# Optimization experiments

Measured on AMD Instinct MI355X. Metric: run time of the kernel, lower is better.

Reference implementation:

```python
import jax, jax.numpy as jnp
import numpy as np

# --- static config (matches init_kwargs / input_specs) ---
N_GRAPHS = 32
NODES = 1000          # num_nodes per graph
N = N_GRAPHS * NODES  # 32000 total nodes
F_IN = 128            # num_features
E_DIM = 16            # edge_attr_dim
H, C = 4, 16          # heads, GAT_dim
HC = H * C            # 64
E = 512000            # edges (before self-loops)
PROJ = 8              # proj_nodes
OUT = 256             # output_dim
NEG_SLOPE = 0.2       # PyG GATConv default


def setup_inputs() -> dict:
    key = jax.random.key(0)
    ks = jax.random.split(key, 20)
    s = 0.1
    return {
        "x": jax.random.normal(ks[0], (N, F_IN), jnp.float32),
        "edge_attr": jax.random.normal(ks[1], (E, E_DIM), jnp.float32),
        # layer 0 (input_conv): F_IN -> H*C
        "W0":   jax.random.normal(ks[2], (F_IN, HC), jnp.float32) * s,
        "a_s0": jax.random.normal(ks[3], (H, C), jnp.float32) * s,
        "a_d0": jax.random.normal(ks[4], (H, C), jnp.float32) * s,
        "W_e0": jax.random.normal(ks[5], (E_DIM, HC), jnp.float32) * s,
        "a_e0": jax.random.normal(ks[6], (H, C), jnp.float32) * s,
        "b0":   jnp.zeros((HC,), jnp.float32),
        # layers 1..2 stacked: HC -> H*C
        "Wg":   jax.random.normal(ks[7], (2, HC, HC), jnp.float32) * s,
        "a_sg": jax.random.normal(ks[8], (2, H, C), jnp.float32) * s,
        "a_dg": jax.random.normal(ks[9], (2, H, C), jnp.float32) * s,
        "W_eg": jax.random.normal(ks[10], (2, E_DIM, HC), jnp.float32) * s,
        "a_eg": jax.random.normal(ks[11], (2, H, C), jnp.float32) * s,
        "bg":   jnp.zeros((2, HC), jnp.float32),
        # node_proj: HC -> PROJ ; fc_out: NODES*PROJ -> OUT
        "Wp": jax.random.normal(ks[12], (HC, PROJ), jnp.float32) * s,
        "bp": jnp.zeros((PROJ,), jnp.float32),
        "Wo": jax.random.normal(ks[13], (NODES * PROJ, OUT), jnp.float32) * (s / 4),
        "bo": jnp.zeros((OUT,), jnp.float32),
        "edge_index": jax.random.randint(ks[14], (2, E), 0, N, jnp.int32),
        "batch": jnp.repeat(jnp.arange(N_GRAPHS, dtype=jnp.int32), NODES),
    }


def _gat_layer(x, src, dst, eattr, W, a_s, a_d, W_e, a_e, b):
    """PyG GATConv (concat=True, shared src/dst lin, edge_dim) forward."""
    xl = (x @ W).reshape(N, H, C)                       # [N,H,C]
    al_s = jnp.sum(xl * a_s, axis=-1)                   # [N,H]
    al_d = jnp.sum(xl * a_d, axis=-1)                   # [N,H]
    el = (eattr @ W_e).reshape(-1, H, C)                # [Ef,H,C]
    al_e = jnp.sum(el * a_e, axis=-1)                   # [Ef,H]
    logits = jax.nn.leaky_relu(al_s[src] + al_d[dst] + al_e, NEG_SLOPE)
    # segment softmax over destination nodes (every node has a self-loop)
    mx = jax.ops.segment_max(logits, dst, num_segments=N)
    p = jnp.exp(logits - mx[dst])
    denom = jax.ops.segment_sum(p, dst, num_segments=N)
    alpha = p / denom[dst]                               # [Ef,H]
    out = jax.ops.segment_sum(xl[src] * alpha[..., None], dst, num_segments=N)
    return out.reshape(N, HC) + b


def reference(x, edge_attr, W0, a_s0, a_d0, W_e0, a_e0, b0,
              Wg, a_sg, a_dg, W_eg, a_eg, bg,
              Wp, bp, Wo, bo, edge_index, batch):
    src, dst = edge_index[0], edge_index[1]
    # PyG add_self_loops with fill_value='mean': per-dst mean of incoming edge_attr
    deg = jax.ops.segment_sum(jnp.ones((E,), edge_attr.dtype), dst, num_segments=N)
    loop_attr = jax.ops.segment_sum(edge_attr, dst, num_segments=N) / jnp.maximum(deg, 1.0)[:, None]
    loops = jnp.arange(N, dtype=src.dtype)
    src_f = jnp.concatenate([src, loops])
    dst_f = jnp.concatenate([dst, loops])
    ea_f = jnp.concatenate([edge_attr, loop_attr], axis=0)   # [E+N, E_DIM]

    h = jax.nn.relu(_gat_layer(x, src_f, dst_f, ea_f, W0, a_s0, a_d0, W_e0, a_e0, b0))
    for i in range(2):
        h = jax.nn.relu(_gat_layer(h, src_f, dst_f, ea_f,
                                   Wg[i], a_sg[i], a_dg[i], W_eg[i], a_eg[i], bg[i]))
    h = jax.nn.relu(h @ Wp + bp)                             # [N, PROJ]
    B = batch.shape[0] // NODES                              # static batch count
    h = h.reshape(B, NODES * PROJ)
    return h @ Wo + bo                                       # [B, OUT]
```

## Files before the change

kernel.cpp:

```cpp
#include <hip/hip_runtime.h>
#include <hip/hip_bf16.h>

#define N_NODES 32000
#define FIN     128
#define E_EDGES 512000
#define EF_EDGES 544000
#define HC      64
#define NGRAPH  32
#define PROJ    8
#define OUT_DIM 256

static __device__ inline unsigned short f2bf(float f) {
  unsigned int x = __float_as_uint(f);
  unsigned int r = (x + 0x7fffu + ((x >> 16) & 1u)) >> 16;
  return (unsigned short)r;
}
static __device__ inline float bf2f(unsigned short u) {
  return __uint_as_float((unsigned int)u << 16);
}

__global__ __launch_bounds__(256) void deg_kernel(const int* __restrict__ ei,
                                                  int* __restrict__ deg) {
  int e = blockIdx.x * 256 + threadIdx.x;
  atomicAdd(&deg[ei[E_EDGES + e]], 1);
}

__global__ __launch_bounds__(1024) void scan_kernel(const int* __restrict__ deg,
                                                    int* __restrict__ offs,
                                                    int* __restrict__ nxt) {
  __shared__ int part[1024];
  int t = threadIdx.x;
  int base = t * 32;
  int local[32];
  int s = 0;
#pragma unroll
  for (int i = 0; i < 32; ++i) {
    int idx = base + i;
    int v = (idx < N_NODES) ? (deg[idx] + 1) : 0;
    local[i] = s;
    s += v;
  }
  part[t] = s;
  __syncthreads();
  for (int off = 1; off < 1024; off <<= 1) {
    int v = (t >= off) ? part[t - off] : 0;
    __syncthreads();
    part[t] += v;
    __syncthreads();
  }
  int pre = (t > 0) ? part[t - 1] : 0;
#pragma unroll
  for (int i = 0; i < 32; ++i) {
    int idx = base + i;
    if (idx < N_NODES) {
      int o = pre + local[i];
      offs[idx] = o;
      nxt[idx] = o;
    }
  }
  if (t == 1023) offs[N_NODES] = part[1023];
}

__global__ __launch_bounds__(256) void fill_kernel(const int* __restrict__ ei,
                                                   int* __restrict__ nxt,
                                                   int* __restrict__ csr_src,
                                                   int* __restrict__ csr_eid,
                                                   int* __restrict__ csr_pos) {
  int e = blockIdx.x * 256 + threadIdx.x;
  int s, d;
  if (e < E_EDGES) { s = ei[e]; d = ei[E_EDGES + e]; }
  else             { s = e - E_EDGES; d = s; }
  int pos = atomicAdd(&nxt[d], 1);
  csr_src[pos] = s;
  csr_eid[pos] = e;
  csr_pos[e] = pos;
}

__global__ __launch_bounds__(256) void loopattr_kernel(const int* __restrict__ offs,
                                                       const int* __restrict__ csr_eid,
                                                       const float* __restrict__ ea,
                                                       float* __restrict__ loop_attr) {
  int lane = threadIdx.x & 63;
  int n = blockIdx.x * 4 + (threadIdx.x >> 6);
  int k = lane & 15, g = lane >> 4;
  int beg = offs[n], end = offs[n + 1];
  float s = 0.f;
  for (int i = beg + g; i < end; i += 4) {
    int e = csr_eid[i];
    if (e < E_EDGES) s += ea[(size_t)e * 16 + k];
  }
  s += __shfl_xor(s, 16);
  s += __shfl_xor(s, 32);
  int degv = end - beg - 1;
  if (g == 0) loop_attr[(size_t)n * 16 + k] = s / fmaxf((float)degv, 1.f);
}

template <int K>
__global__ __launch_bounds__(256) void transform_kernel(const float* __restrict__ A,
                                                        const float* __restrict__ W,
                                                        const float* __restrict__ a_s,
                                                        const float* __restrict__ a_d,
                                                        unsigned short* __restrict__ xlb,
                                                        float* __restrict__ al_s,
                                                        float* __restrict__ al_d) {
  __shared__ float sW[64][64];
  __shared__ float sA[64][65];
  int tid = threadIdx.x;
  int row0 = blockIdx.x * 64;
  int tx = tid & 15, ty = tid >> 4;
  int c0 = tx * 4, r0 = ty * 4;
  float acc[4][4] = {};
  for (int kc = 0; kc < K; kc += 64) {
    for (int i = tid; i < 1024; i += 256) {
      int kk = i >> 4, c4 = (i & 15) * 4;
      *(float4*)&sW[kk][c4] = *(const float4*)&W[(size_t)(kc + kk) * HC + c4];
    }
    for (int i = tid; i < 1024; i += 256) {
      int r = i >> 4, k4 = (i & 15) * 4;
      float4 v = *(const float4*)&A[(size_t)(row0 + r) * K + kc + k4];
      sA[r][k4 + 0] = v.x; sA[r][k4 + 1] = v.y;
      sA[r][k4 + 2] = v.z; sA[r][k4 + 3] = v.w;
    }
    __syncthreads();
#pragma unroll 8
    for (int kk = 0; kk < 64; ++kk) {
      float4 w = *(float4*)&sW[kk][c0];
      float a0 = sA[r0 + 0][kk];
      float a1 = sA[r0 + 1][kk];
      float a2 = sA[r0 + 2][kk];
      float a3 = sA[r0 + 3][kk];
      acc[0][0] = fmaf(a0, w.x, acc[0][0]); acc[0][1] = fmaf(a0, w.y, acc[0][1]);
      acc[0][2] = fmaf(a0, w.z, acc[0][2]); acc[0][3] = fmaf(a0, w.w, acc[0][3]);
      acc[1][0] = fmaf(a1, w.x, acc[1][0]); acc[1][1] = fmaf(a1, w.y, acc[1][1]);
      acc[1][2] = fmaf(a1, w.z, acc[1][2]); acc[1][3] = fmaf(a1, w.w, acc[1][3]);
      acc[2][0] = fmaf(a2, w.x, acc[2][0]); acc[2][1] = fmaf(a2, w.y, acc[2][1]);
      acc[2][2] = fmaf(a2, w.z, acc[2][2]); acc[2][3] = fmaf(a2, w.w, acc[2][3]);
      acc[3][0] = fmaf(a3, w.x, acc[3][0]); acc[3][1] = fmaf(a3, w.y, acc[3][1]);
      acc[3][2] = fmaf(a3, w.z, acc[3][2]); acc[3][3] = fmaf(a3, w.w, acc[3][3]);
    }
    __syncthreads();
  }
  float asv[4], adv[4];
#pragma unroll
  for (int j = 0; j < 4; ++j) { asv[j] = a_s[c0 + j]; adv[j] = a_d[c0 + j]; }
  int hd = tx >> 2;
#pragma unroll
  for (int i = 0; i < 4; ++i) {
    int r = row0 + r0 + i;
    ushort4 u = make_ushort4(f2bf(acc[i][0]), f2bf(acc[i][1]),
                             f2bf(acc[i][2]), f2bf(acc[i][3]));
    *(ushort4*)&xlb[(size_t)r * HC + c0] = u;
    float ps = acc[i][0] * asv[0] + acc[i][1] * asv[1] + acc[i][2] * asv[2] + acc[i][3] * asv[3];
    float pd = acc[i][0] * adv[0] + acc[i][1] * adv[1] + acc[i][2] * adv[2] + acc[i][3] * adv[3];
    ps += __shfl_xor(ps, 1); ps += __shfl_xor(ps, 2);
    pd += __shfl_xor(pd, 1); pd += __shfl_xor(pd, 2);
    if ((tx & 3) == 0) {
      al_s[(size_t)r * 4 + hd] = ps;
      al_d[(size_t)r * 4 + hd] = pd;
    }
  }
}

__global__ __launch_bounds__(256) void logit_kernel(const float* __restrict__ edge_attr,
                                                    const float* __restrict__ loop_attr,
                                                    const float* __restrict__ W_e,
                                                    const float* __restrict__ a_e,
                                                    const int* __restrict__ ei,
                                                    const int* __restrict__ csr_pos,
                                                    const float* __restrict__ al_s,
                                                    float* __restrict__ lg0) {
  __shared__ float sMe[16][4];
  int tid = threadIdx.x;
  if (tid < 64) {
    int d = tid >> 2, h = tid & 3;
    float s = 0.f;
#pragma unroll
    for (int c = 0; c < 16; ++c) s += W_e[d * HC + h * 16 + c] * a_e[h * 16 + c];
    sMe[d][h] = s;
  }
  __syncthreads();
  int e = blockIdx.x * 256 + tid;
  int src;
  const float* ea;
  if (e < E_EDGES) { src = ei[e];          ea = &edge_attr[(size_t)e * 16]; }
  else             { src = e - E_EDGES;    ea = &loop_attr[(size_t)(e - E_EDGES) * 16]; }
  float4 v0 = *(const float4*)(ea + 0);
  float4 v1 = *(const float4*)(ea + 4);
  float4 v2 = *(const float4*)(ea + 8);
  float4 v3 = *(const float4*)(ea + 12);
  float4 als = *(const float4*)&al_s[(size_t)src * 4];
  float r[4];
#pragma unroll
  for (int h = 0; h < 4; ++h) {
    r[h] = v0.x * sMe[0][h] + v0.y * sMe[1][h] + v0.z * sMe[2][h] + v0.w * sMe[3][h] +
           v1.x * sMe[4][h] + v1.y * sMe[5][h] + v1.z * sMe[6][h] + v1.w * sMe[7][h] +
           v2.x * sMe[8][h] + v2.y * sMe[9][h] + v2.z * sMe[10][h] + v2.w * sMe[11][h] +
           v3.x * sMe[12][h] + v3.y * sMe[13][h] + v3.z * sMe[14][h] + v3.w * sMe[15][h];
  }
  int pos = csr_pos[e];
  *(float4*)&lg0[(size_t)pos * 4] =
      make_float4(r[0] + als.x, r[1] + als.y, r[2] + als.z, r[3] + als.w);
}

template <int FUSE_PROJ>
__global__ __launch_bounds__(256) void gather_kernel(const int* __restrict__ offs,
                                                     const int* __restrict__ csr_src,
                                                     const float* __restrict__ lg0,
                                                     const unsigned short* __restrict__ xlb,
                                                     const float* __restrict__ al_d,
                                                     const float* __restrict__ bias,
                                                     const float* __restrict__ Wp,
                                                     const float* __restrict__ bp,
                                                     float* __restrict__ outp) {
  int lane = threadIdx.x & 63;
  int n = blockIdx.x * 4 + (threadIdx.x >> 6);
  int hd = lane >> 4;
  int beg = offs[n], end = offs[n + 1];
  float ald = al_d[(size_t)n * 4 + hd];
  float m = -1e30f, denom = 0.f, acc = 0.f;
  int i = beg;
  for (; i + 4 <= end; i += 4) {
    int s0 = csr_src[i + 0];
    int s1 = csr_src[i + 1];
    int s2 = csr_src[i + 2];
    int s3 = csr_src[i + 3];
    float l0 = lg0[(size_t)(i + 0) * 4 + hd] + ald;
    float l1 = lg0[(size_t)(i + 1) * 4 + hd] + ald;
    float l2 = lg0[(size_t)(i + 2) * 4 + hd] + ald;
    float l3 = lg0[(size_t)(i + 3) * 4 + hd] + ald;
    l0 = (l0 > 0.f) ? l0 : 0.2f * l0;
    l1 = (l1 > 0.f) ? l1 : 0.2f * l1;
    l2 = (l2 > 0.f) ? l2 : 0.2f * l2;
    l3 = (l3 > 0.f) ? l3 : 0.2f * l3;
    unsigned short x0 = xlb[(size_t)s0 * HC + lane];
    unsigned short x1 = xlb[(size_t)s1 * HC + lane];
    unsigned short x2 = xlb[(size_t)s2 * HC + lane];
    unsigned short x3 = xlb[(size_t)s3 * HC + lane];
    float mx = fmaxf(fmaxf(fmaxf(l0, l1), fmaxf(l2, l3)), m);
    float sc = __expf(m - mx);
    float p0 = __expf(l0 - mx);
    float p1 = __expf(l1 - mx);
    float p2 = __expf(l2 - mx);
    float p3 = __expf(l3 - mx);
    denom = denom * sc + ((p0 + p1) + (p2 + p3));
    acc = acc * sc + p0 * bf2f(x0) + p1 * bf2f(x1) + p2 * bf2f(x2) + p3 * bf2f(x3);
    m = mx;
  }
  for (; i < end; ++i) {
    int s = csr_src[i];
    float l = lg0[(size_t)i * 4 + hd] + ald;
    l = (l > 0.f) ? l : 0.2f * l;
    float mx = fmaxf(m, l);
    float sc = __expf(m - mx);
    float p = __expf(l - mx);
    denom = denom * sc + p;
    acc = acc * sc + p * bf2f(xlb[(size_t)s * HC + lane]);
    m = mx;
  }
  float hv = fmaxf(acc / denom + bias[lane], 0.f);
  if constexpr (!FUSE_PROJ) {
    outp[(size_t)n * HC + lane] = hv;
  } else {
    float pj[8];
#pragma unroll
    for (int j = 0; j < 8; ++j) pj[j] = hv * Wp[lane * PROJ + j];
#pragma unroll
    for (int off = 1; off < 64; off <<= 1) {
#pragma unroll
      for (int j = 0; j < 8; ++j) pj[j] += __shfl_xor(pj[j], off);
    }
    if (lane < 8) {
      float v = pj[0];
      v = (lane == 1) ? pj[1] : v;
      v = (lane == 2) ? pj[2] : v;
      v = (lane == 3) ? pj[3] : v;
      v = (lane == 4) ? pj[4] : v;
      v = (lane == 5) ? pj[5] : v;
      v = (lane == 6) ? pj[6] : v;
      v = (lane == 7) ? pj[7] : v;
      outp[(size_t)n * PROJ + lane] = fmaxf(v + bp[lane], 0.f);
    }
  }
}

__global__ __launch_bounds__(256) void fc1_kernel(const float* __restrict__ p,
                                                  const float* __restrict__ Wo,
                                                  float* __restrict__ part) {
  __shared__ float sp[NGRAPH][250];
  int kc = blockIdx.x;
  int ct = blockIdx.y;
  int tid = threadIdx.x;
  for (int i = tid; i < NGRAPH * 250; i += 256) {
    int g = i / 250, kk = i % 250;
    sp[g][kk] = p[(size_t)g * 8000 + kc * 250 + kk];
  }
  __syncthreads();
  int c = ct * 64 + (tid & 63);
  int kg = tid >> 6;
  float acc[NGRAPH] = {};
  for (int kk = kg; kk < 250; kk += 4) {
    float w = Wo[(size_t)(kc * 250 + kk) * OUT_DIM + c];
#pragma unroll
    for (int g = 0; g < NGRAPH; ++g) acc[g] = fmaf(sp[g][kk], w, acc[g]);
  }
  int ch = kc * 4 + kg;
#pragma unroll
  for (int g = 0; g < NGRAPH; ++g)
    part[((size_t)ch * NGRAPH + g) * OUT_DIM + c] = acc[g];
}

__global__ __launch_bounds__(256) void fc2_kernel(const float* __restrict__ part,
                                                  const float* __restrict__ bo,
                                                  float* __restrict__ out) {
  int i = blockIdx.x * 256 + threadIdx.x;
  int g = i >> 8, c = i & 255;
  float s = bo[c];
  for (int ch = 0; ch < 128; ++ch) s += part[((size_t)ch * NGRAPH + g) * OUT_DIM + c];
  out[i] = s;
}

extern "C" void kernel_launch(void* const* d_in, const int* in_sizes, int n_in,
                              void* d_out, int out_size, void* d_ws, size_t ws_size,
                              hipStream_t stream) {
  const float* x         = (const float*)d_in[0];
  const float* edge_attr = (const float*)d_in[1];
  const float* W0        = (const float*)d_in[2];
  const float* a_s0      = (const float*)d_in[3];
  const float* a_d0      = (const float*)d_in[4];
  const float* W_e0      = (const float*)d_in[5];
  const float* a_e0      = (const float*)d_in[6];
  const float* b0        = (const float*)d_in[7];
  const float* Wg        = (const float*)d_in[8];
  const float* a_sg      = (const float*)d_in[9];
  const float* a_dg      = (const float*)d_in[10];
  const float* W_eg      = (const float*)d_in[11];
  const float* a_eg      = (const float*)d_in[12];
  const float* bg        = (const float*)d_in[13];
  const float* Wp        = (const float*)d_in[14];
  const float* bp        = (const float*)d_in[15];
  const float* Wo        = (const float*)d_in[16];
  const float* bo        = (const float*)d_in[17];
  const int*   ei        = (const int*)d_in[18];

  char* base = (char*)d_ws;
  size_t off = 0;
  auto alloc = [&](size_t bytes) -> void* {
    void* ptr = base + off;
    off = (off + bytes + 255) & ~(size_t)255;
    return ptr;
  };
  int*            deg       = (int*)alloc((size_t)N_NODES * 4);
  int*            offs      = (int*)alloc((size_t)(N_NODES + 1) * 4);
  int*            nxt       = (int*)alloc((size_t)N_NODES * 4);
  int*            csr_src   = (int*)alloc((size_t)EF_EDGES * 4);
  int*            csr_eid   = (int*)alloc((size_t)EF_EDGES * 4);
  int*            csr_pos   = (int*)alloc((size_t)EF_EDGES * 4);
  float*          loop_attr = (float*)alloc((size_t)N_NODES * 16 * 4);
  float*          lg0       = (float*)alloc((size_t)EF_EDGES * 4 * 4);
  unsigned short* xlb       = (unsigned short*)alloc((size_t)N_NODES * HC * 2);
  float*          al_s      = (float*)alloc((size_t)N_NODES * 4 * 4);
  float*          al_d      = (float*)alloc((size_t)N_NODES * 4 * 4);
  float*          hA        = (float*)alloc((size_t)N_NODES * HC * 4);
  float*          hB        = (float*)alloc((size_t)N_NODES * HC * 4);
  float*          pbuf      = (float*)alloc((size_t)N_NODES * PROJ * 4);
  float*          part      = (float*)alloc((size_t)128 * NGRAPH * OUT_DIM * 4);

  hipMemsetAsync(deg, 0, (size_t)N_NODES * 4, stream);
  deg_kernel<<<E_EDGES / 256, 256, 0, stream>>>(ei, deg);
  scan_kernel<<<1, 1024, 0, stream>>>(deg, offs, nxt);
  fill_kernel<<<EF_EDGES / 256, 256, 0, stream>>>(ei, nxt, csr_src, csr_eid, csr_pos);
  loopattr_kernel<<<N_NODES / 4, 256, 0, stream>>>(offs, csr_eid, edge_attr, loop_attr);

  transform_kernel<FIN><<<N_NODES / 64, 256, 0, stream>>>(x, W0, a_s0, a_d0, xlb, al_s, al_d);
  logit_kernel<<<EF_EDGES / 256, 256, 0, stream>>>(edge_attr, loop_attr, W_e0, a_e0, ei, csr_pos, al_s, lg0);
  gather_kernel<0><<<N_NODES / 4, 256, 0, stream>>>(offs, csr_src, lg0, xlb, al_d, b0, Wp, bp, hA);

  transform_kernel<HC><<<N_NODES / 64, 256, 0, stream>>>(hA, Wg, a_sg, a_dg, xlb, al_s, al_d);
  logit_kernel<<<EF_EDGES / 256, 256, 0, stream>>>(edge_attr, loop_attr, W_eg, a_eg, ei, csr_pos, al_s, lg0);
  gather_kernel<0><<<N_NODES / 4, 256, 0, stream>>>(offs, csr_src, lg0, xlb, al_d, bg, Wp, bp, hB);

  transform_kernel<HC><<<N_NODES / 64, 256, 0, stream>>>(hB, Wg + HC * HC, a_sg + 64, a_dg + 64, xlb, al_s, al_d);
  logit_kernel<<<EF_EDGES / 256, 256, 0, stream>>>(edge_attr, loop_attr, W_eg + 16 * HC, a_eg + 64, ei, csr_pos, al_s, lg0);
  gather_kernel<1><<<N_NODES / 4, 256, 0, stream>>>(offs, csr_src, lg0, xlb, al_d, bg + 64, Wp, bp, pbuf);

  fc1_kernel<<<dim3(32, 4), 256, 0, stream>>>(pbuf, Wo, part);
  fc2_kernel<<<NGRAPH, 256, 0, stream>>>(part, bo, (float*)d_out);
}
```

Baseline: 320.9 us.

## Replace single-block prefix scan with three-pass multi-block wave-shuffle scan

The single 1024-thread block that computed the degree prefix sum (32 serial elements per thread plus a shared-memory Hillis-Steele scan) is replaced by three kernels. A multi-block pass does wave-shuffle scans per 256-element chunk, one small block scans the 125 block sums, and a final pass adds the block offsets and writes offs and nxt. This spreads the scan across many CUs and removes the uncoalesced strided loads. In exchange it adds two kernel launches and two tiny workspace buffers.

```diff
diff --git a/kernel.cpp b/kernel.cpp
--- a/kernel.cpp
+++ b/kernel.cpp
@@ -25,40 +25,58 @@
   atomicAdd(&deg[ei[E_EDGES + e]], 1);
 }
 
-__global__ __launch_bounds__(1024) void scan_kernel(const int* __restrict__ deg,
+__global__ __launch_bounds__(256) void scan1_kernel(const int* __restrict__ deg,
+                                                    int* __restrict__ offs,
+                                                    int* __restrict__ bsum) {
+  int idx = blockIdx.x * 256 + threadIdx.x;
+  int lane = threadIdx.x & 63;
+  int w = threadIdx.x >> 6;
+  int v = deg[idx] + 1;
+  int s = v;
+#pragma unroll
+  for (int off = 1; off < 64; off <<= 1) {
+    int t = __shfl_up(s, off);
+    if (lane >= off) s += t;
+  }
+  __shared__ int wsum[4];
+  if (lane == 63) wsum[w] = s;
+  __syncthreads();
+  int add = 0;
+#pragma unroll
+  for (int i = 0; i < 4; ++i) add += (i < w) ? wsum[i] : 0;
+  int incl = s + add;
+  offs[idx] = incl - v;
+  if (threadIdx.x == 255) bsum[blockIdx.x] = incl;
+}
+
+__global__ __launch_bounds__(128) void scan2_kernel(const int* __restrict__ bsum,
+                                                    int* __restrict__ boffs,
+                                                    int* __restrict__ offs) {
+  int t = threadIdx.x;
+  int lane = t & 63;
+  int w = t >> 6;
+  int v = (t < 125) ? bsum[t] : 0;
+  int s = v;
+#pragma unroll
+  for (int off = 1; off < 64; off <<= 1) {
+    int tt = __shfl_up(s, off);
+    if (lane >= off) s += tt;
+  }
+  __shared__ int wsum[2];
+  if (lane == 63) wsum[w] = s;
+  __syncthreads();
+  int incl = s + ((w == 1) ? wsum[0] : 0);
+  if (t < 125) boffs[t] = incl - v;
+  if (t == 127) offs[N_NODES] = incl;
+}
+
+__global__ __launch_bounds__(256) void scan3_kernel(const int* __restrict__ boffs,
                                                     int* __restrict__ offs,
                                                     int* __restrict__ nxt) {
-  __shared__ int part[1024];
-  int t = threadIdx.x;
-  int base = t * 32;
-  int local[32];
-  int s = 0;
-#pragma unroll
-  for (int i = 0; i < 32; ++i) {
-    int idx = base + i;
-    int v = (idx < N_NODES) ? (deg[idx] + 1) : 0;
-    local[i] = s;
-    s += v;
-  }
-  part[t] = s;
-  __syncthreads();
-  for (int off = 1; off < 1024; off <<= 1) {
-    int v = (t >= off) ? part[t - off] : 0;
-    __syncthreads();
-    part[t] += v;
-    __syncthreads();
-  }
-  int pre = (t > 0) ? part[t - 1] : 0;
-#pragma unroll
-  for (int i = 0; i < 32; ++i) {
-    int idx = base + i;
-    if (idx < N_NODES) {
-      int o = pre + local[i];
-      offs[idx] = o;
-      nxt[idx] = o;
-    }
-  }
-  if (t == 1023) offs[N_NODES] = part[1023];
+  int idx = blockIdx.x * 256 + threadIdx.x;
+  int o = offs[idx] + boffs[blockIdx.x];
+  offs[idx] = o;
+  nxt[idx] = o;
 }
 
 __global__ __launch_bounds__(256) void fill_kernel(const int* __restrict__ ei,
@@ -352,6 +370,8 @@
   int*            deg       = (int*)alloc((size_t)N_NODES * 4);
   int*            offs      = (int*)alloc((size_t)(N_NODES + 1) * 4);
   int*            nxt       = (int*)alloc((size_t)N_NODES * 4);
+  int*            bsum      = (int*)alloc(128 * 4);
+  int*            boffs     = (int*)alloc(128 * 4);
   int*            csr_src   = (int*)alloc((size_t)EF_EDGES * 4);
   int*            csr_eid   = (int*)alloc((size_t)EF_EDGES * 4);
   int*            csr_pos   = (int*)alloc((size_t)EF_EDGES * 4);
@@ -367,7 +387,9 @@
 
   hipMemsetAsync(deg, 0, (size_t)N_NODES * 4, stream);
   deg_kernel<<<E_EDGES / 256, 256, 0, stream>>>(ei, deg);
-  scan_kernel<<<1, 1024, 0, stream>>>(deg, offs, nxt);
+  scan1_kernel<<<N_NODES / 256, 256, 0, stream>>>(deg, offs, bsum);
+  scan2_kernel<<<1, 128, 0, stream>>>(bsum, boffs, offs);
+  scan3_kernel<<<N_NODES / 256, 256, 0, stream>>>(boffs, offs, nxt);
   fill_kernel<<<EF_EDGES / 256, 256, 0, stream>>>(ei, nxt, csr_src, csr_eid, csr_pos);
   loopattr_kernel<<<N_NODES / 4, 256, 0, stream>>>(offs, csr_eid, edge_attr, loop_attr);
 
```

Result: faster. 278.8 us (-13.1%).
